# Performance work log

Measured on AMD Instinct MI355X. Metric: run time of the kernel, lower is better.

Reference implementation:

```python
import jax, jax.numpy as jnp
import numpy as np

# DeepSeek-V2 MLA dims (one tensor-parallel shard of 8)
H = 5120          # hidden size
S = 2048          # seq len
B = 1
NH = 16           # 128 heads / 8 devices
Q_LORA = 1536
KV_LORA = 512
NOPE = 128
ROPE = 64
QK = NOPE + ROPE  # 192 per-head q/k dim
VD = 128          # v head dim
DEVICE_NUM = 8
EPS = 1e-6


def rms_norm(x, w):
    v = jnp.mean(jnp.square(x.astype(jnp.float32)), axis=-1, keepdims=True)
    return (x * jax.lax.rsqrt(v + EPS)).astype(x.dtype) * w


def rope_cos_sin(position_ids, dim=ROPE, base=10000.0):
    inv_freq = 1.0 / (base ** (jnp.arange(0, dim, 2, dtype=jnp.float32) / dim))
    freqs = position_ids.astype(jnp.float32)[..., None] * inv_freq       # [B,S,dim/2]
    emb = jnp.concatenate([freqs, freqs], axis=-1)                        # [B,S,dim]
    return jnp.cos(emb), jnp.sin(emb)


def apply_rope(x, cos, sin):
    # DeepSeek interleaved reorder: view(b,h,s,d//2,2).transpose(-1,-2).reshape
    b, h, s, d = x.shape
    x = x.reshape(b, h, s, d // 2, 2).transpose(0, 1, 2, 4, 3).reshape(b, h, s, d)
    x1, x2 = x[..., : d // 2], x[..., d // 2:]
    rot = jnp.concatenate([-x2, x1], axis=-1)
    return x * cos[:, None] + rot * sin[:, None]


def setup_inputs() -> dict:
    key = jax.random.key(0)
    ks = jax.random.split(key, 8)
    sc = 0.02
    hidden_states = jax.random.normal(ks[0], (B, S, H), dtype=jnp.float32)
    position_ids = jnp.arange(S, dtype=jnp.int64 if jax.config.jax_enable_x64 else jnp.int32)[None, :].repeat(B, 0)
    attention_mask = jnp.triu(jnp.full((S, S), -1e9, dtype=jnp.float32), 1)[None, None]
    return {
        "hidden_states": hidden_states,
        "position_ids": position_ids,
        "attention_mask": attention_mask,
        "ln_w": jnp.ones((H,), jnp.float32),
        "q_a_w": jax.random.normal(ks[1], (Q_LORA, H), jnp.float32) * sc,
        "q_a_ln_w": jnp.ones((Q_LORA,), jnp.float32),
        "q_b_w": jax.random.normal(ks[2], (NH * QK, Q_LORA), jnp.float32) * sc,
        "kv_a_w": jax.random.normal(ks[3], (KV_LORA + ROPE, H), jnp.float32) * sc,
        "kv_a_ln_w": jnp.ones((KV_LORA,), jnp.float32),
        "kv_b_w": jax.random.normal(ks[4], (NH * (NOPE + VD), KV_LORA), jnp.float32) * sc,
        "o_w": jax.random.normal(ks[5], (H, NH * VD), jnp.float32) * sc,
    }


def reference(hidden_states, position_ids, attention_mask, ln_w, q_a_w, q_a_ln_w,
              q_b_w, kv_a_w, kv_a_ln_w, kv_b_w, o_w):
    b, s, _ = hidden_states.shape
    residual = hidden_states * (1.0 / DEVICE_NUM)
    x = rms_norm(hidden_states, ln_w)

    # Q path: low-rank down-proj + RMSNorm + up-proj
    q = rms_norm(x @ q_a_w.T, q_a_ln_w) @ q_b_w.T                # [b,s,NH*QK]
    q = q.reshape(b, s, NH, QK).transpose(0, 2, 1, 3)            # [b,NH,s,QK]
    q_nope, q_pe = q[..., :NOPE], q[..., NOPE:]

    # KV path: compressed latent + shared rope key
    ckv = x @ kv_a_w.T                                           # [b,s,KV_LORA+ROPE]
    c_kv, k_pe = ckv[..., :KV_LORA], ckv[..., KV_LORA:]
    k_pe = k_pe.reshape(b, s, 1, ROPE).transpose(0, 2, 1, 3)     # [b,1,s,ROPE]
    kv = rms_norm(c_kv, kv_a_ln_w) @ kv_b_w.T                    # [b,s,NH*(NOPE+VD)]
    kv = kv.reshape(b, s, NH, NOPE + VD).transpose(0, 2, 1, 3)
    k_nope, v = kv[..., :NOPE], kv[..., NOPE:]

    cos, sin = rope_cos_sin(position_ids)
    q_pe = apply_rope(q_pe, cos, sin)
    k_pe = apply_rope(k_pe, cos, sin)

    k = jnp.concatenate([k_nope, jnp.broadcast_to(k_pe, (b, NH, s, ROPE))], axis=-1)
    qf = jnp.concatenate([q_nope, q_pe], axis=-1)

    scores = jnp.einsum('bhqd,bhkd->bhqk', qf, k) * (1.0 / np.sqrt(QK))
    scores = scores + attention_mask
    probs = jax.nn.softmax(scores, axis=-1)
    attn = jnp.einsum('bhqk,bhkd->bhqd', probs, v)               # [b,NH,s,VD]

    out = attn.transpose(0, 2, 1, 3).reshape(b, s, NH * VD) @ o_w.T
    hidden = residual + out
    return hidden.astype(jnp.float32), k.astype(jnp.float32), v.astype(jnp.float32)
```

## Files before the change

kernel.cpp:

```cpp
#include <hip/hip_runtime.h>
#include <math.h>

typedef unsigned short u16;
typedef unsigned int u32;
typedef __attribute__((ext_vector_type(8))) short short8;
typedef __attribute__((ext_vector_type(4))) float f32x4;

#define NHEADS 16
static const int S      = 2048;
static const int Hd     = 5120;
static const int QLORA  = 1536;
static const int KVLORA = 512;
static const int NQK    = 192;
static const int NVD    = 128;
static const int QDIM   = 3072;
static const int KVDIM  = 4096;
static const int NFUSE  = 2176;

__device__ __forceinline__ u16 f2bf(float f) {
    union { float f; u32 u; } v; v.f = f;
    u32 r = v.u + 0x7FFFu + ((v.u >> 16) & 1u);
    return (u16)(r >> 16);
}
__device__ __forceinline__ float bf2f(u16 h) {
    union { u32 u; float f; } v; v.u = (u32)h << 16; return v.f;
}

__global__ void convert_bf16_kernel(const float* __restrict__ src, u16* __restrict__ dst,
                                    int n_src, int n_total) {
    int i = (blockIdx.x * 256 + threadIdx.x) * 4;
    if (i >= n_total) return;
    union { u16 h[4]; uint2 u; } p;
    if (i < n_src) {
        float4 v = *(const float4*)(src + i);
        p.h[0] = f2bf(v.x); p.h[1] = f2bf(v.y); p.h[2] = f2bf(v.z); p.h[3] = f2bf(v.w);
    } else {
        p.h[0] = p.h[1] = p.h[2] = p.h[3] = 0;
    }
    *(uint2*)(dst + i) = p.u;
}

__global__ void rmsnorm_bf16_kernel(const float* in, const float* __restrict__ w,
                                    u16* out, int D, int in_stride, int out_stride) {
    int row = blockIdx.x;
    const float* x = in + (size_t)row * in_stride;
    u16* y = out + (size_t)row * out_stride;
    float ss = 0.f;
    for (int i = threadIdx.x; i < D; i += blockDim.x) { float v = x[i]; ss += v * v; }
    #pragma unroll
    for (int off = 32; off > 0; off >>= 1) ss += __shfl_xor(ss, off);
    __shared__ float wsum[8];
    int wid = threadIdx.x >> 6, lane = threadIdx.x & 63;
    if (lane == 0) wsum[wid] = ss;
    __syncthreads();
    float tot = 0.f;
    int nw = blockDim.x >> 6;
    for (int i = 0; i < nw; ++i) tot += wsum[i];
    float scale = rsqrtf(tot / (float)D + 1e-6f);
    for (int i = threadIdx.x; i < D; i += blockDim.x) y[i] = f2bf(x[i] * scale * w[i]);
}

__global__ void rmsnorm_bf16in_kernel(const u16* in, const float* __restrict__ w,
                                      u16* out, int D, int in_stride, int out_stride) {
    int row = blockIdx.x;
    const u16* x = in + (size_t)row * in_stride;
    u16* y = out + (size_t)row * out_stride;
    float ss = 0.f;
    for (int i = threadIdx.x; i < D; i += blockDim.x) { float v = bf2f(x[i]); ss += v * v; }
    #pragma unroll
    for (int off = 32; off > 0; off >>= 1) ss += __shfl_xor(ss, off);
    __shared__ float wsum[8];
    int wid = threadIdx.x >> 6, lane = threadIdx.x & 63;
    if (lane == 0) wsum[wid] = ss;
    __syncthreads();
    float tot = 0.f;
    int nw = blockDim.x >> 6;
    for (int i = 0; i < nw; ++i) tot += wsum[i];
    float scale = rsqrtf(tot / (float)D + 1e-6f);
    for (int i = threadIdx.x; i < D; i += blockDim.x) y[i] = f2bf(bf2f(x[i]) * scale * w[i]);
}

template<int BM, bool SWZ, bool OBF, bool QPERM>
__global__ __launch_bounds__(256) void gemm_k(
    const u16* __restrict__ A, const u16* __restrict__ B, void* __restrict__ Cv,
    int M, int N, int K, const float* __restrict__ resid) {
    constexpr int MR = BM / 32;
    __shared__ u16 As[4][BM * 32];
    __shared__ u16 Bs[4][128 * 32];

    int bm, bn;
    if constexpr (SWZ) {
        const int lin = blockIdx.x + blockIdx.y * gridDim.x;
        const int nwg = gridDim.x * gridDim.y;
        const int xcd = lin & 7, off = lin >> 3;
        const int q = nwg >> 3, r = nwg & 7;
        const int wg = (xcd < r ? xcd * (q + 1) : r * (q + 1) + (xcd - r) * q) + off;
        bm = (wg % gridDim.y) * BM;
        bn = (wg / gridDim.y) * 128;
    } else {
        bm = blockIdx.y * BM;
        bn = blockIdx.x * 128;
    }

    const int tid = threadIdx.x;
    const int w = tid >> 6, lane = tid & 63;
    const int wr = w >> 1, wc = w & 1;
    const int fr = lane & 15, kg = lane >> 4;

    f32x4 acc[MR][4];
    #pragma unroll
    for (int i = 0; i < MR; ++i)
        #pragma unroll
        for (int j = 0; j < 4; ++j) acc[i][j] = (f32x4){0.f, 0.f, 0.f, 0.f};

    const int srow = lane >> 2;
    const int scol = (lane & 3) * 8;
    const u16* Ap0 = A + (size_t)(bm + w * (BM / 4) + srow) * K + scol;
    const u16* Ap1 = Ap0 + (size_t)16 * K;
    const u16* Bp0 = B + (size_t)(bn + w * 32 + srow) * K + scol;
    const u16* Bp1 = Bp0 + (size_t)16 * K;
    const int lda0 = (w * (BM / 4)) * 32;
    const int lda1 = (w * (BM / 4) + 16) * 32;
    const int ldb0 = (w * 32) * 32;
    const int ldb1 = (w * 32 + 16) * 32;

    auto STAGE = [&](int buf, int kk) {
        __builtin_amdgcn_global_load_lds(
            (const __attribute__((address_space(1))) void*)(Ap0 + kk),
            (__attribute__((address_space(3))) void*)&As[buf][lda0], 16, 0, 0);
        if constexpr (BM == 128)
            __builtin_amdgcn_global_load_lds(
                (const __attribute__((address_space(1))) void*)(Ap1 + kk),
                (__attribute__((address_space(3))) void*)&As[buf][lda1], 16, 0, 0);
        __builtin_amdgcn_global_load_lds(
            (const __attribute__((address_space(1))) void*)(Bp0 + kk),
            (__attribute__((address_space(3))) void*)&Bs[buf][ldb0], 16, 0, 0);
        __builtin_amdgcn_global_load_lds(
            (const __attribute__((address_space(1))) void*)(Bp1 + kk),
            (__attribute__((address_space(3))) void*)&Bs[buf][ldb1], 16, 0, 0);
    };
    auto COMP = [&](int buf) {
        short8 af[MR], bfr[4];
        #pragma unroll
        for (int i = 0; i < MR; ++i)
            af[i] = *(const short8*)&As[buf][(wr * (BM / 2) + i * 16 + fr) * 32 + kg * 8];
        #pragma unroll
        for (int i = 0; i < 4; ++i)
            bfr[i] = *(const short8*)&Bs[buf][(wc * 64 + i * 16 + fr) * 32 + kg * 8];
        #pragma unroll
        for (int mi = 0; mi < MR; ++mi)
            #pragma unroll
            for (int ni = 0; ni < 4; ++ni)
                acc[mi][ni] = __builtin_amdgcn_mfma_f32_16x16x32_bf16(af[mi], bfr[ni],
                                                                      acc[mi][ni], 0, 0, 0);
    };

    const int nk = K >> 5;
    STAGE(0, 0);
    STAGE(1, 32);
    for (int kt = 0; kt < nk; ++kt) {
        if (kt + 2 < nk) {
            STAGE((kt + 2) & 3, (kt + 2) << 5);
            if constexpr (BM == 128) asm volatile("s_waitcnt vmcnt(8)" ::: "memory");
            else                     asm volatile("s_waitcnt vmcnt(6)" ::: "memory");
        } else if (kt + 1 < nk) {
            if constexpr (BM == 128) asm volatile("s_waitcnt vmcnt(4)" ::: "memory");
            else                     asm volatile("s_waitcnt vmcnt(3)" ::: "memory");
        } else {
            asm volatile("s_waitcnt vmcnt(0)" ::: "memory");
        }
        __builtin_amdgcn_s_barrier();
        COMP(kt & 3);
    }

    #pragma unroll
    for (int mi = 0; mi < MR; ++mi)
        #pragma unroll
        for (int ni = 0; ni < 4; ++ni)
            #pragma unroll
            for (int r2 = 0; r2 < 4; ++r2) {
                int row = bm + wr * (BM / 2) + mi * 16 + kg * 4 + r2;
                int col = bn + wc * 64 + ni * 16 + fr;
                float v = acc[mi][ni][r2];
                if constexpr (QPERM) {
                    size_t idx = ((size_t)(col / 192) * S + row) * 192 + (col % 192);
                    ((u16*)Cv)[idx] = f2bf(v);
                } else if constexpr (OBF) {
                    ((u16*)Cv)[(size_t)row * N + col] = f2bf(v);
                } else {
                    size_t idx = (size_t)row * N + col;
                    if (resid) v += resid[idx] * 0.125f;
                    ((float*)Cv)[idx] = v;
                }
            }
}

__global__ void rope_q_inplace_kernel(u16* __restrict__ Qbf, const int* __restrict__ pos) {
    const int s = blockIdx.x;
    const int t = threadIdx.x;
    const int hh = t >> 5, j = t & 31;
    float ps = (float)pos[s];
    float inv_freq = 1.0f / powf(10000.0f, (float)j * (1.0f / 32.0f));
    float ang = ps * inv_freq;
    float c = cosf(ang), sn = sinf(ang);
    u16* base = Qbf + ((size_t)hh * S + s) * NQK;
    float a = bf2f(base[128 + 2 * j]), b = bf2f(base[128 + 2 * j + 1]);
    __syncthreads();
    base[128 + j] = f2bf(a * c - b * sn);
    base[160 + j] = f2bf(b * c + a * sn);
}

__global__ __launch_bounds__(256) void build_kv64_kernel(
    const u16* __restrict__ KVb, const u16* __restrict__ CF,
    const int* __restrict__ pos_ids,
    float* __restrict__ Kout, float* __restrict__ Vout,
    u16* __restrict__ Kbf, u16* __restrict__ Vtb) {
    const int s0 = blockIdx.x * 64;
    const int h  = blockIdx.y;
    const int t  = threadIdx.x;
    __shared__ u16 T[64][132];

    #pragma unroll
    for (int it = 0; it < 4; ++it) {
        int i = t + it * 256;
        int row = i >> 4, c8 = (i & 15) * 8;
        int s = s0 + row;
        union { uint4 u; u16 hx[8]; } v;
        v.u = *(const uint4*)(KVb + (size_t)s * KVDIM + h * 256 + c8);
        size_t kidx = ((size_t)h * S + s) * NQK + c8;
        *(uint4*)(Kbf + kidx) = v.u;
        float4 f0 = {bf2f(v.hx[0]), bf2f(v.hx[1]), bf2f(v.hx[2]), bf2f(v.hx[3])};
        float4 f1 = {bf2f(v.hx[4]), bf2f(v.hx[5]), bf2f(v.hx[6]), bf2f(v.hx[7])};
        *(float4*)(Kout + kidx) = f0;
        *(float4*)(Kout + kidx + 4) = f1;
    }
    #pragma unroll
    for (int it = 0; it < 4; ++it) {
        int i = t + it * 256;
        int row = i >> 4, c8 = (i & 15) * 8;
        int s = s0 + row;
        union { uint4 u; uint2 d[2]; u16 hx[8]; } v;
        v.u = *(const uint4*)(KVb + (size_t)s * KVDIM + h * 256 + 128 + c8);
        *(uint2*)&T[row][c8]     = v.d[0];
        *(uint2*)&T[row][c8 + 4] = v.d[1];
        size_t vidx = ((size_t)h * S + s) * NVD + c8;
        float4 f0 = {bf2f(v.hx[0]), bf2f(v.hx[1]), bf2f(v.hx[2]), bf2f(v.hx[3])};
        float4 f1 = {bf2f(v.hx[4]), bf2f(v.hx[5]), bf2f(v.hx[6]), bf2f(v.hx[7])};
        *(float4*)(Vout + vidx) = f0;
        *(float4*)(Vout + vidx + 4) = f1;
    }
    #pragma unroll
    for (int it = 0; it < 8; ++it) {
        int i = t + it * 256;
        int row = i >> 5, j = i & 31;
        int s = s0 + row;
        float ps = (float)pos_ids[s];
        float inv_freq = 1.0f / powf(10000.0f, (float)j * (1.0f / 32.0f));
        float ang = ps * inv_freq;
        float c = cosf(ang), sn = sinf(ang);
        u32 pr = *(const u32*)(CF + (size_t)s * NFUSE + QLORA + KVLORA + 2 * j);
        float a = bf2f((u16)pr), b = bf2f((u16)(pr >> 16));
        float k0 = a * c - b * sn;
        float k1 = b * c + a * sn;
        size_t kidx = ((size_t)h * S + s) * NQK;
        Kout[kidx + 128 + j] = k0;
        Kout[kidx + 160 + j] = k1;
        Kbf[kidx + 128 + j] = f2bf(k0);
        Kbf[kidx + 160 + j] = f2bf(k1);
    }
    __syncthreads();
    const int d = t >> 1, half = t & 1;
    #pragma unroll
    for (int c = 0; c < 4; ++c) {
        u16 tmp[8];
        #pragma unroll
        for (int e = 0; e < 8; ++e) tmp[e] = T[half * 32 + c * 8 + e][d];
        *(uint4*)(Vtb + ((size_t)h * NVD + d) * S + s0 + half * 32 + c * 8) = *(uint4*)tmp;
    }
}

__global__ __launch_bounds__(256) void attn_mfma_kernel(
    const u16* __restrict__ Qbf, const u16* __restrict__ Kb,
    const u16* __restrict__ Vtb, u16* __restrict__ ATb) {
    const int h = blockIdx.y;
    const int q0 = (gridDim.x - 1 - blockIdx.x) * 64;
    const int tid = threadIdx.x;
    const int w = tid >> 6, lane = tid & 63;
    const int fr = lane & 15, kg = lane >> 4;

    __shared__ __align__(16) u16 Ks[2][64 * 192];
    __shared__ __align__(16) u16 Vts[2][128 * 64];

    int kSrc[6], vSrc[4];
    #pragma unroll
    for (int i = 0; i < 6; ++i) {
        int D = (w * 6 + i) * 1024 + lane * 16;
        int row = D / 384, wb = D - row * 384;
        kSrc[i] = row * 384 + (wb ^ ((row & 7) << 4));
    }
    #pragma unroll
    for (int i = 0; i < 4; ++i) {
        int D = (w * 4 + i) * 1024 + lane * 16;
        int row = D >> 7, wb = D & 127;
        vSrc[i] = row * (S * 2) + (wb ^ ((row & 7) << 4));
    }
    const char* Kg = (const char*)(Kb + (size_t)h * S * NQK);
    const char* Vg = (const char*)(Vtb + (size_t)h * NVD * S);

    auto STAGE = [&](int buf, int kt) {
        const size_t krow = (size_t)kt * 64;
        #pragma unroll
        for (int i = 0; i < 6; ++i)
            __builtin_amdgcn_global_load_lds(
                (const __attribute__((address_space(1))) void*)(Kg + krow * 384 + kSrc[i]),
                (__attribute__((address_space(3))) void*)((char*)&Ks[buf][0] + (w * 6 + i) * 1024), 16, 0, 0);
        #pragma unroll
        for (int i = 0; i < 4; ++i)
            __builtin_amdgcn_global_load_lds(
                (const __attribute__((address_space(1))) void*)(Vg + krow * 2 + vSrc[i]),
                (__attribute__((address_space(3))) void*)((char*)&Vts[buf][0] + (w * 4 + i) * 1024), 16, 0, 0);
    };

    short8 qf[6];
    {
        const u16* qrow = Qbf + ((size_t)h * S + q0 + w * 16 + fr) * NQK;
        #pragma unroll
        for (int kb = 0; kb < 6; ++kb)
            qf[kb] = *(const short8*)(qrow + kb * 32 + kg * 8);
    }

    f32x4 o[8];
    #pragma unroll
    for (int ni = 0; ni < 8; ++ni) o[ni] = (f32x4){0.f, 0.f, 0.f, 0.f};
    float mrow = -1e30f, lrow = 0.f;
    const float scale = 0.0721687836487032f;
    const int qg = q0 + w * 16 + fr;
    const int swz = (fr & 7) << 4;
    const int nt = (q0 >> 6) + 1;

    STAGE(0, 0);
    asm volatile("s_waitcnt vmcnt(0)" ::: "memory");
    __builtin_amdgcn_s_barrier();

    for (int t = 0; t < nt; ++t) {
        if (t + 1 < nt) STAGE((t + 1) & 1, t + 1);
        const int buf = t & 1;
        const int k0 = t * 64;

        f32x4 sacc[4];
        #pragma unroll
        for (int mi = 0; mi < 4; ++mi) sacc[mi] = (f32x4){0.f, 0.f, 0.f, 0.f};
        __builtin_amdgcn_s_setprio(1);
        #pragma unroll
        for (int mi = 0; mi < 4; ++mi)
            #pragma unroll
            for (int kb = 0; kb < 6; ++kb) {
                const short8 kf = *(const short8*)((const char*)&Ks[buf][0] +
                    (mi * 16 + fr) * 384 + ((kb * 64 + kg * 16) ^ swz));
                sacc[mi] = __builtin_amdgcn_mfma_f32_16x16x32_bf16(kf, qf[kb], sacc[mi], 0, 0, 0);
            }
        __builtin_amdgcn_s_setprio(0);

        const bool diag = (k0 == q0);
        float p[4][4];
        float mx = -1e30f;
        #pragma unroll
        for (int mi = 0; mi < 4; ++mi)
            #pragma unroll
            for (int r = 0; r < 4; ++r) {
                float v = sacc[mi][r] * scale;
                if (diag && (k0 + mi * 16 + kg * 4 + r > qg)) v = -1e30f;
                p[mi][r] = v;
                mx = fmaxf(mx, v);
            }
        mx = fmaxf(mx, __shfl_xor(mx, 16));
        mx = fmaxf(mx, __shfl_xor(mx, 32));
        float mnew = fmaxf(mrow, mx);
        float corr = __expf(mrow - mnew);
        float psum = 0.f;
        #pragma unroll
        for (int mi = 0; mi < 4; ++mi)
            #pragma unroll
            for (int r = 0; r < 4; ++r) {
                float e = __expf(p[mi][r] - mnew);
                p[mi][r] = e;
                psum += e;
            }
        psum += __shfl_xor(psum, 16);
        psum += __shfl_xor(psum, 32);
        lrow = lrow * corr + psum;
        mrow = mnew;
        float corr_r[4];
        #pragma unroll
        for (int r = 0; r < 4; ++r) corr_r[r] = __shfl(corr, kg * 4 + r);
        #pragma unroll
        for (int ni = 0; ni < 8; ++ni) {
            o[ni][0] *= corr_r[0]; o[ni][1] *= corr_r[1];
            o[ni][2] *= corr_r[2]; o[ni][3] *= corr_r[3];
        }

        u32 pk0[4], pk1[4];
        #pragma unroll
        for (int mi = 0; mi < 4; ++mi) {
            pk0[mi] = (u32)f2bf(p[mi][0]) | ((u32)f2bf(p[mi][1]) << 16);
            pk1[mi] = (u32)f2bf(p[mi][2]) | ((u32)f2bf(p[mi][3]) << 16);
        }
        const int srcA = 2 * (kg & 1) * 16 + fr;
        const int srcB = srcA + 16;
        const int hsel = kg >> 1;
        short8 pa[2];
        #pragma unroll
        for (int ks = 0; ks < 2; ++ks) {
            u32 a0 = (u32)__shfl((int)pk0[ks * 2], srcA), b0 = (u32)__shfl((int)pk0[ks * 2 + 1], srcA);
            u32 a1 = (u32)__shfl((int)pk1[ks * 2], srcA), b1 = (u32)__shfl((int)pk1[ks * 2 + 1], srcA);
            u32 a2 = (u32)__shfl((int)pk0[ks * 2], srcB), b2 = (u32)__shfl((int)pk0[ks * 2 + 1], srcB);
            u32 a3 = (u32)__shfl((int)pk1[ks * 2], srcB), b3 = (u32)__shfl((int)pk1[ks * 2 + 1], srcB);
            union { u32 u[4]; short8 s8; } cvt;
            cvt.u[0] = hsel ? b0 : a0;
            cvt.u[1] = hsel ? b1 : a1;
            cvt.u[2] = hsel ? b2 : a2;
            cvt.u[3] = hsel ? b3 : a3;
            pa[ks] = cvt.s8;
        }

        __builtin_amdgcn_s_setprio(1);
        #pragma unroll
        for (int ks = 0; ks < 2; ++ks)
            #pragma unroll
            for (int ni = 0; ni < 8; ++ni) {
                const short8 vf = *(const short8*)((const char*)&Vts[buf][0] +
                    (ni * 16 + fr) * 128 + ((ks * 64 + kg * 16) ^ swz));
                o[ni] = __builtin_amdgcn_mfma_f32_16x16x32_bf16(pa[ks], vf, o[ni], 0, 0, 0);
            }
        __builtin_amdgcn_s_setprio(0);

        asm volatile("s_waitcnt vmcnt(0)" ::: "memory");
        __builtin_amdgcn_s_barrier();
    }

    float inv = 1.f / lrow;
    float inv_r[4];
    #pragma unroll
    for (int r = 0; r < 4; ++r) inv_r[r] = __shfl(inv, kg * 4 + r);
    u16* outp = ATb + (size_t)(q0 + w * 16 + kg * 4) * (NHEADS * NVD) + h * NVD + fr;
    #pragma unroll
    for (int ni = 0; ni < 8; ++ni)
        #pragma unroll
        for (int r = 0; r < 4; ++r)
            outp[(size_t)r * (NHEADS * NVD) + ni * 16] = f2bf(o[ni][r] * inv_r[r]);
}

extern "C" void kernel_launch(void* const* d_in, const int* in_sizes, int n_in,
                              void* d_out, int out_size, void* d_ws, size_t ws_size,
                              hipStream_t stream) {
    (void)in_sizes; (void)n_in; (void)out_size; (void)ws_size;
    const float* hidden    = (const float*)d_in[0];
    const int*   pos       = (const int*)d_in[1];
    const float* ln_w      = (const float*)d_in[3];
    const float* q_a_w     = (const float*)d_in[4];
    const float* q_a_ln_w  = (const float*)d_in[5];
    const float* q_b_w     = (const float*)d_in[6];
    const float* kv_a_w    = (const float*)d_in[7];
    const float* kv_a_ln_w = (const float*)d_in[8];
    const float* kv_b_w    = (const float*)d_in[9];
    const float* o_w       = (const float*)d_in[10];

    float* OUT_H = (float*)d_out;
    float* OUT_K = OUT_H + (size_t)S * Hd;
    float* OUT_V = OUT_K + (size_t)NHEADS * S * NQK;

    char* ws = (char*)d_ws;
    u16*   o_wb    = (u16*)(ws);
    u16*   Wf      = (u16*)(ws + 20971520);
    u16*   Qbf     = (u16*)(ws + 20971520);
    u16*   Vtb     = (u16*)(ws + 33554432);
    u16*   Xb      = (u16*)(ws + 43253760);
    u16*   Kbf     = (u16*)(ws + 43253760);
    u16*   ATb     = (u16*)(ws + 55836672);
    u16*   CF      = (u16*)(ws + 64225280);
    u16*   QAn     = (u16*)(ws + 73138176);
    u16*   CKVN    = (u16*)(ws + 73138176);
    u16*   q_b_wb  = (u16*)(ws + 79429632);
    u16*   kv_b_wb = (u16*)(ws + 79429632);
    u16*   KVb     = (u16*)(ws + 88866816);

    convert_bf16_kernel<<<(Hd * 2048 / 4 + 255) / 256, 256, 0, stream>>>(o_w, o_wb, Hd * 2048, Hd * 2048);
    convert_bf16_kernel<<<(QLORA * Hd / 4 + 255) / 256, 256, 0, stream>>>(q_a_w, Wf, QLORA * Hd, QLORA * Hd);
    convert_bf16_kernel<<<(640 * Hd / 4 + 255) / 256, 256, 0, stream>>>(kv_a_w, Wf + (size_t)QLORA * Hd, 576 * Hd, 640 * Hd);

    rmsnorm_bf16_kernel<<<S, 256, 0, stream>>>(hidden, ln_w, Xb, Hd, Hd, Hd);
    gemm_k<128, true, true, false><<<dim3(NFUSE / 128, S / 128), 256, 0, stream>>>(Xb, Wf, CF, S, NFUSE, Hd, nullptr);
    convert_bf16_kernel<<<(QDIM * QLORA / 4 + 255) / 256, 256, 0, stream>>>(q_b_w, q_b_wb, QDIM * QLORA, QDIM * QLORA);
    rmsnorm_bf16in_kernel<<<S, 256, 0, stream>>>(CF, q_a_ln_w, QAn, QLORA, NFUSE, QLORA);
    gemm_k<128, true, true, true><<<dim3(QDIM / 128, S / 128), 256, 0, stream>>>(QAn, q_b_wb, Qbf, S, QDIM, QLORA, nullptr);
    rope_q_inplace_kernel<<<S, 512, 0, stream>>>(Qbf, pos);
    convert_bf16_kernel<<<(KVDIM * KVLORA / 4 + 255) / 256, 256, 0, stream>>>(kv_b_w, kv_b_wb, KVDIM * KVLORA, KVDIM * KVLORA);
    rmsnorm_bf16in_kernel<<<S, 256, 0, stream>>>(CF + QLORA, kv_a_ln_w, CKVN, KVLORA, NFUSE, KVLORA);
    gemm_k<64, false, true, false><<<dim3(KVDIM / 128, S / 64), 256, 0, stream>>>(CKVN, kv_b_wb, KVb, S, KVDIM, KVLORA, nullptr);
    build_kv64_kernel<<<dim3(S / 64, NHEADS), 256, 0, stream>>>(KVb, CF, pos, OUT_K, OUT_V, Kbf, Vtb);
    attn_mfma_kernel<<<dim3(S / 64, NHEADS), 256, 0, stream>>>(Qbf, Kbf, Vtb, ATb);
    gemm_k<64, false, false, false><<<dim3(Hd / 128, S / 64), 256, 0, stream>>>(ATb, o_wb, OUT_H, S, Hd, NHEADS * NVD, hidden);
}
```

Measured before the change: 418.5 us.

## Use 256x256-tile 8-wave GEMM with interleaved LDS prefetch for output projection

Replaces the 64x128-tile GEMM for the o_proj with a new 512-thread kernel that computes 256x256 output tiles. It uses direct global-to-LDS loads into swizzled double buffers, split into four parts that are interleaved with four MFMA phases and raise wave priority around the MFMAs. The larger tiles give more reuse per byte loaded and overlap loads with compute. With only 20x8=160 blocks the grid is small for the device's CU count, so occupancy and tail effects are a risk, and the higher register use per thread adds pressure.

```diff
diff --git a/kernel.cpp b/kernel.cpp
--- a/kernel.cpp
+++ b/kernel.cpp
@@ -195,6 +195,112 @@
             }
 }
 
+#define QUAD8(MI, NI, A0, A1)                                                                 \
+    acc[MI][NI] = __builtin_amdgcn_mfma_f32_16x16x32_bf16(A0, bf[NI][0], acc[MI][NI], 0, 0, 0); \
+    acc[MI][NI] = __builtin_amdgcn_mfma_f32_16x16x32_bf16(A1, bf[NI][1], acc[MI][NI], 0, 0, 0);
+
+#define PHASE8(BUF, MI0) do {                                                                 \
+    const int ra0 = wr * 128 + (MI0) * 16 + fr;                                               \
+    const int ra1 = ra0 + 16;                                                                 \
+    short8 a00 = *(const short8*)((const char*)&As[BUF][0] + ra0 * 128 + ((kg * 16) ^ swz));  \
+    short8 a01 = *(const short8*)((const char*)&As[BUF][0] + ra0 * 128 + ((64 + kg * 16) ^ swz)); \
+    short8 a10 = *(const short8*)((const char*)&As[BUF][0] + ra1 * 128 + ((kg * 16) ^ swz));  \
+    short8 a11 = *(const short8*)((const char*)&As[BUF][0] + ra1 * 128 + ((64 + kg * 16) ^ swz)); \
+    __builtin_amdgcn_s_setprio(1);                                                            \
+    QUAD8(MI0, 0, a00, a01) QUAD8(MI0, 1, a00, a01)                                           \
+    QUAD8(MI0, 2, a00, a01) QUAD8(MI0, 3, a00, a01)                                           \
+    QUAD8(MI0 + 1, 0, a10, a11) QUAD8(MI0 + 1, 1, a10, a11)                                   \
+    QUAD8(MI0 + 1, 2, a10, a11) QUAD8(MI0 + 1, 3, a10, a11)                                   \
+    __builtin_amdgcn_s_setprio(0);                                                            \
+  } while (0)
+
+#define G8STAGE(BUF, KT, PART) do {                                                           \
+    const u16* Gp = ((PART) >= 2) ? A : B;                                                    \
+    const int hh = (PART) & 1;                                                                \
+    const int br = (((PART) >= 2) ? bm : bn) + hh * 128;                                      \
+    const char* gb = (const char*)(Gp + (size_t)br * K + (KT) * 64);                          \
+    u16* lb = ((PART) >= 2) ? &As[BUF][0] : &Bs[BUF][0];                                      \
+    __builtin_amdgcn_global_load_lds(                                                         \
+        (const __attribute__((address_space(1))) void*)(gb + (size_t)r0 * K2 + c0),           \
+        (__attribute__((address_space(3))) void*)((char*)lb + hh * 16384 + w * 1024), 16, 0, 0); \
+    __builtin_amdgcn_global_load_lds(                                                         \
+        (const __attribute__((address_space(1))) void*)(gb + (size_t)r1 * K2 + c1),           \
+        (__attribute__((address_space(3))) void*)((char*)lb + hh * 16384 + 8192 + w * 1024), 16, 0, 0); \
+  } while (0)
+
+__global__ __launch_bounds__(512, 2) void gemm8_kernel(
+    const u16* __restrict__ A, const u16* __restrict__ B, float* __restrict__ C,
+    int M, int N, int K, const float* __restrict__ resid) {
+    __shared__ u16 As[2][256 * 64];
+    __shared__ u16 Bs[2][256 * 64];
+    const int bm = blockIdx.y * 256, bn = blockIdx.x * 256;
+    const int tid = threadIdx.x;
+    const int w = tid >> 6, lane = tid & 63;
+    const int wr = w >> 2, wc = w & 3;
+    const int fr = lane & 15, kg = lane >> 4;
+    const int swz = (fr & 7) << 4;
+
+    f32x4 acc[8][4];
+    #pragma unroll
+    for (int i = 0; i < 8; ++i)
+        #pragma unroll
+        for (int j = 0; j < 4; ++j) acc[i][j] = (f32x4){0.f, 0.f, 0.f, 0.f};
+
+    const int D0 = tid * 16, D1 = 8192 + tid * 16;
+    const int r0 = D0 >> 7; const int c0 = (D0 & 127) ^ ((r0 & 7) << 4);
+    const int r1 = D1 >> 7; const int c1 = (D1 & 127) ^ ((r1 & 7) << 4);
+    const size_t K2 = (size_t)K * 2;
+
+    const int nk = K >> 6;
+    G8STAGE(0, 0, 0); G8STAGE(0, 0, 1); G8STAGE(0, 0, 2); G8STAGE(0, 0, 3);
+
+    short8 bf[4][2];
+    for (int kt = 0; kt < nk; ++kt) {
+        const int b = kt & 1;
+        const bool pre = (kt + 1 < nk);
+        asm volatile("" ::: "memory");
+        if (pre) {
+            G8STAGE(b ^ 1, kt + 1, 0);
+            asm volatile("s_waitcnt vmcnt(2)" ::: "memory");
+        } else {
+            asm volatile("s_waitcnt vmcnt(0)" ::: "memory");
+        }
+        __builtin_amdgcn_s_barrier();
+        asm volatile("" ::: "memory");
+        #pragma unroll
+        for (int ni = 0; ni < 4; ++ni) {
+            const int rb = wc * 64 + ni * 16 + fr;
+            bf[ni][0] = *(const short8*)((const char*)&Bs[b][0] + rb * 128 + ((kg * 16) ^ swz));
+            bf[ni][1] = *(const short8*)((const char*)&Bs[b][0] + rb * 128 + ((64 + kg * 16) ^ swz));
+        }
+        if (pre) G8STAGE(b ^ 1, kt + 1, 1);
+        PHASE8(b, 0);
+        __builtin_amdgcn_s_barrier();
+        if (pre) G8STAGE(b ^ 1, kt + 1, 2);
+        PHASE8(b, 2);
+        __builtin_amdgcn_s_barrier();
+        if (pre) G8STAGE(b ^ 1, kt + 1, 3);
+        PHASE8(b, 4);
+        __builtin_amdgcn_s_barrier();
+        PHASE8(b, 6);
+        __builtin_amdgcn_s_barrier();
+    }
+
+    #pragma unroll
+    for (int mi = 0; mi < 8; ++mi)
+        #pragma unroll
+        for (int ni = 0; ni < 4; ++ni)
+            #pragma unroll
+            for (int r2 = 0; r2 < 4; ++r2) {
+                int row = bm + wr * 128 + mi * 16 + kg * 4 + r2;
+                int col = bn + wc * 64 + ni * 16 + fr;
+                size_t idx = (size_t)row * N + col;
+                float v = acc[mi][ni][r2];
+                if (resid) v += resid[idx] * 0.125f;
+                C[idx] = v;
+            }
+}
+
 __global__ void rope_q_inplace_kernel(u16* __restrict__ Qbf, const int* __restrict__ pos) {
     const int s = blockIdx.x;
     const int t = threadIdx.x;
@@ -499,5 +605,5 @@
     gemm_k<64, false, true, false><<<dim3(KVDIM / 128, S / 64), 256, 0, stream>>>(CKVN, kv_b_wb, KVb, S, KVDIM, KVLORA, nullptr);
     build_kv64_kernel<<<dim3(S / 64, NHEADS), 256, 0, stream>>>(KVb, CF, pos, OUT_K, OUT_V, Kbf, Vtb);
     attn_mfma_kernel<<<dim3(S / 64, NHEADS), 256, 0, stream>>>(Qbf, Kbf, Vtb, ATb);
-    gemm_k<64, false, false, false><<<dim3(Hd / 128, S / 64), 256, 0, stream>>>(ATb, o_wb, OUT_H, S, Hd, NHEADS * NVD, hidden);
-}
+    gemm8_kernel<<<dim3(Hd / 256, S / 256), 512, 0, stream>>>(ATb, o_wb, OUT_H, S, Hd, NHEADS * NVD, hidden);
+}
```

New measurement: 443.4 us. 1.06x slower.

## Merge weight conversions, q/kv rmsnorms, and q/kv up-projection GEMMs into single launches

Applied to the files above, without the earlier changes.

Replaces five separate fp32-to-bf16 weight conversion launches with one kernel that dispatches on a flat chunk index, and merges the q and kv latent RMSNorms into one 2D-grid launch. The q_b and kv_b up-projection GEMMs become one grouped kernel, where blocks with x<24 compute Q and the rest compute KV, all using 64-row tiles. Workspace offsets are moved so CKVN, q_b_wb, kv_b_wb and KVb no longer alias, which lets the merged work coexist. The aim is to cut launch count and tail underutilisation from the small GEMMs. The cost is that the Q GEMM drops from a swizzled 128-row tile to an unswizzled 64-row tile, which may lower its efficiency.

```diff
diff --git a/kernel.cpp b/kernel.cpp
--- a/kernel.cpp
+++ b/kernel.cpp
@@ -26,18 +26,29 @@
     union { u32 u; float f; } v; v.u = (u32)h << 16; return v.f;
 }
 
-__global__ void convert_bf16_kernel(const float* __restrict__ src, u16* __restrict__ dst,
-                                    int n_src, int n_total) {
-    int i = (blockIdx.x * 256 + threadIdx.x) * 4;
-    if (i >= n_total) return;
+__global__ void convert_all_kernel(const float* __restrict__ o_w,
+                                   const float* __restrict__ q_a_w,
+                                   const float* __restrict__ kv_a_w,
+                                   const float* __restrict__ q_b_w,
+                                   const float* __restrict__ kv_b_w,
+                                   u16* __restrict__ o_wb, u16* __restrict__ Wf,
+                                   u16* __restrict__ q_b_wb, u16* __restrict__ kv_b_wb) {
+    long c = (long)blockIdx.x * 256 + threadIdx.x;
+    const float* src; u16* dst; long nsrcc;
+    if (c < 2621440L)      { src = o_w;    dst = o_wb;            nsrcc = 2621440L; }
+    else if (c < 4587520L) { c -= 2621440L; src = q_a_w; dst = Wf; nsrcc = 1966080L; }
+    else if (c < 5406720L) { c -= 4587520L; src = kv_a_w; dst = Wf + 7864320L; nsrcc = 737280L; }
+    else if (c < 6586368L) { c -= 5406720L; src = q_b_w;  dst = q_b_wb;  nsrcc = 1179648L; }
+    else if (c < 7110656L) { c -= 6586368L; src = kv_b_w; dst = kv_b_wb; nsrcc = 524288L; }
+    else return;
     union { u16 h[4]; uint2 u; } p;
-    if (i < n_src) {
-        float4 v = *(const float4*)(src + i);
+    if (c < nsrcc) {
+        float4 v = *(const float4*)(src + c * 4);
         p.h[0] = f2bf(v.x); p.h[1] = f2bf(v.y); p.h[2] = f2bf(v.z); p.h[3] = f2bf(v.w);
     } else {
         p.h[0] = p.h[1] = p.h[2] = p.h[3] = 0;
     }
-    *(uint2*)(dst + i) = p.u;
+    *(uint2*)(dst + c * 4) = p.u;
 }
 
 __global__ void rmsnorm_bf16_kernel(const float* in, const float* __restrict__ w,
@@ -60,22 +71,27 @@
     for (int i = threadIdx.x; i < D; i += blockDim.x) y[i] = f2bf(x[i] * scale * w[i]);
 }
 
-__global__ void rmsnorm_bf16in_kernel(const u16* in, const float* __restrict__ w,
-                                      u16* out, int D, int in_stride, int out_stride) {
-    int row = blockIdx.x;
-    const u16* x = in + (size_t)row * in_stride;
-    u16* y = out + (size_t)row * out_stride;
+__global__ void rms_qkv_kernel(const u16* __restrict__ CF,
+                               const float* __restrict__ qw, const float* __restrict__ kw,
+                               u16* __restrict__ QAn, u16* __restrict__ CKVN) {
+    const int row = blockIdx.x;
+    const u16* x; u16* y; const float* w; int D;
+    if (blockIdx.y == 0) {
+        x = CF + (size_t)row * NFUSE;          y = QAn + (size_t)row * QLORA;
+        w = qw; D = QLORA;
+    } else {
+        x = CF + (size_t)row * NFUSE + QLORA;  y = CKVN + (size_t)row * KVLORA;
+        w = kw; D = KVLORA;
+    }
     float ss = 0.f;
     for (int i = threadIdx.x; i < D; i += blockDim.x) { float v = bf2f(x[i]); ss += v * v; }
     #pragma unroll
     for (int off = 32; off > 0; off >>= 1) ss += __shfl_xor(ss, off);
-    __shared__ float wsum[8];
+    __shared__ float wsum[4];
     int wid = threadIdx.x >> 6, lane = threadIdx.x & 63;
     if (lane == 0) wsum[wid] = ss;
     __syncthreads();
-    float tot = 0.f;
-    int nw = blockDim.x >> 6;
-    for (int i = 0; i < nw; ++i) tot += wsum[i];
+    float tot = wsum[0] + wsum[1] + wsum[2] + wsum[3];
     float scale = rsqrtf(tot / (float)D + 1e-6f);
     for (int i = threadIdx.x; i < D; i += blockDim.x) y[i] = f2bf(bf2f(x[i]) * scale * w[i]);
 }
@@ -195,6 +211,100 @@
             }
 }
 
+__global__ __launch_bounds__(256) void gemm_qkv_kernel(
+    const u16* __restrict__ QAn, const u16* __restrict__ CKVN,
+    const u16* __restrict__ q_b_wb, const u16* __restrict__ kv_b_wb,
+    u16* __restrict__ Qbf, u16* __restrict__ KVb) {
+    __shared__ u16 As[4][64 * 32];
+    __shared__ u16 Bs[4][128 * 32];
+    const bool isQ = blockIdx.x < 24;
+    const u16* A = isQ ? QAn : CKVN;
+    const u16* B = isQ ? q_b_wb : kv_b_wb;
+    const int K = isQ ? QLORA : KVLORA;
+    const int bn = (isQ ? blockIdx.x : blockIdx.x - 24) * 128;
+    const int bm = blockIdx.y * 64;
+
+    const int tid = threadIdx.x;
+    const int w = tid >> 6, lane = tid & 63;
+    const int wr = w >> 1, wc = w & 1;
+    const int fr = lane & 15, kg = lane >> 4;
+
+    f32x4 acc[2][4];
+    #pragma unroll
+    for (int i = 0; i < 2; ++i)
+        #pragma unroll
+        for (int j = 0; j < 4; ++j) acc[i][j] = (f32x4){0.f, 0.f, 0.f, 0.f};
+
+    const int srow = lane >> 2;
+    const int scol = (lane & 3) * 8;
+    const u16* Ap0 = A + (size_t)(bm + w * 16 + srow) * K + scol;
+    const u16* Bp0 = B + (size_t)(bn + w * 32 + srow) * K + scol;
+    const u16* Bp1 = Bp0 + (size_t)16 * K;
+    const int lda0 = (w * 16) * 32;
+    const int ldb0 = (w * 32) * 32;
+    const int ldb1 = (w * 32 + 16) * 32;
+
+    auto STAGE = [&](int buf, int kk) {
+        __builtin_amdgcn_global_load_lds(
+            (const __attribute__((address_space(1))) void*)(Ap0 + kk),
+            (__attribute__((address_space(3))) void*)&As[buf][lda0], 16, 0, 0);
+        __builtin_amdgcn_global_load_lds(
+            (const __attribute__((address_space(1))) void*)(Bp0 + kk),
+            (__attribute__((address_space(3))) void*)&Bs[buf][ldb0], 16, 0, 0);
+        __builtin_amdgcn_global_load_lds(
+            (const __attribute__((address_space(1))) void*)(Bp1 + kk),
+            (__attribute__((address_space(3))) void*)&Bs[buf][ldb1], 16, 0, 0);
+    };
+    auto COMP = [&](int buf) {
+        short8 af[2], bfr[4];
+        #pragma unroll
+        for (int i = 0; i < 2; ++i)
+            af[i] = *(const short8*)&As[buf][(wr * 32 + i * 16 + fr) * 32 + kg * 8];
+        #pragma unroll
+        for (int i = 0; i < 4; ++i)
+            bfr[i] = *(const short8*)&Bs[buf][(wc * 64 + i * 16 + fr) * 32 + kg * 8];
+        #pragma unroll
+        for (int mi = 0; mi < 2; ++mi)
+            #pragma unroll
+            for (int ni = 0; ni < 4; ++ni)
+                acc[mi][ni] = __builtin_amdgcn_mfma_f32_16x16x32_bf16(af[mi], bfr[ni],
+                                                                      acc[mi][ni], 0, 0, 0);
+    };
+
+    const int nk = K >> 5;
+    STAGE(0, 0);
+    STAGE(1, 32);
+    for (int kt = 0; kt < nk; ++kt) {
+        if (kt + 2 < nk) {
+            STAGE((kt + 2) & 3, (kt + 2) << 5);
+            asm volatile("s_waitcnt vmcnt(6)" ::: "memory");
+        } else if (kt + 1 < nk) {
+            asm volatile("s_waitcnt vmcnt(3)" ::: "memory");
+        } else {
+            asm volatile("s_waitcnt vmcnt(0)" ::: "memory");
+        }
+        __builtin_amdgcn_s_barrier();
+        COMP(kt & 3);
+    }
+
+    #pragma unroll
+    for (int mi = 0; mi < 2; ++mi)
+        #pragma unroll
+        for (int ni = 0; ni < 4; ++ni)
+            #pragma unroll
+            for (int r2 = 0; r2 < 4; ++r2) {
+                int row = bm + wr * 32 + mi * 16 + kg * 4 + r2;
+                int col = bn + wc * 64 + ni * 16 + fr;
+                float v = acc[mi][ni][r2];
+                if (isQ) {
+                    size_t idx = ((size_t)(col / 192) * S + row) * 192 + (col % 192);
+                    Qbf[idx] = f2bf(v);
+                } else {
+                    KVb[(size_t)row * KVDIM + col] = f2bf(v);
+                }
+            }
+}
+
 __global__ void rope_q_inplace_kernel(u16* __restrict__ Qbf, const int* __restrict__ pos) {
     const int s = blockIdx.x;
     const int t = threadIdx.x;
@@ -479,24 +589,18 @@
     u16*   ATb     = (u16*)(ws + 55836672);
     u16*   CF      = (u16*)(ws + 64225280);
     u16*   QAn     = (u16*)(ws + 73138176);
-    u16*   CKVN    = (u16*)(ws + 73138176);
-    u16*   q_b_wb  = (u16*)(ws + 79429632);
-    u16*   kv_b_wb = (u16*)(ws + 79429632);
-    u16*   KVb     = (u16*)(ws + 88866816);
-
-    convert_bf16_kernel<<<(Hd * 2048 / 4 + 255) / 256, 256, 0, stream>>>(o_w, o_wb, Hd * 2048, Hd * 2048);
-    convert_bf16_kernel<<<(QLORA * Hd / 4 + 255) / 256, 256, 0, stream>>>(q_a_w, Wf, QLORA * Hd, QLORA * Hd);
-    convert_bf16_kernel<<<(640 * Hd / 4 + 255) / 256, 256, 0, stream>>>(kv_a_w, Wf + (size_t)QLORA * Hd, 576 * Hd, 640 * Hd);
-
+    u16*   CKVN    = (u16*)(ws + 79429632);
+    u16*   q_b_wb  = (u16*)(ws + 81526784);
+    u16*   kv_b_wb = (u16*)(ws + 90963968);
+    u16*   KVb     = (u16*)(ws + 95158272);
+
+    convert_all_kernel<<<27776, 256, 0, stream>>>(o_w, q_a_w, kv_a_w, q_b_w, kv_b_w,
+                                                  o_wb, Wf, q_b_wb, kv_b_wb);
     rmsnorm_bf16_kernel<<<S, 256, 0, stream>>>(hidden, ln_w, Xb, Hd, Hd, Hd);
     gemm_k<128, true, true, false><<<dim3(NFUSE / 128, S / 128), 256, 0, stream>>>(Xb, Wf, CF, S, NFUSE, Hd, nullptr);
-    convert_bf16_kernel<<<(QDIM * QLORA / 4 + 255) / 256, 256, 0, stream>>>(q_b_w, q_b_wb, QDIM * QLORA, QDIM * QLORA);
-    rmsnorm_bf16in_kernel<<<S, 256, 0, stream>>>(CF, q_a_ln_w, QAn, QLORA, NFUSE, QLORA);
-    gemm_k<128, true, true, true><<<dim3(QDIM / 128, S / 128), 256, 0, stream>>>(QAn, q_b_wb, Qbf, S, QDIM, QLORA, nullptr);
+    rms_qkv_kernel<<<dim3(S, 2), 256, 0, stream>>>(CF, q_a_ln_w, kv_a_ln_w, QAn, CKVN);
+    gemm_qkv_kernel<<<dim3(56, S / 64), 256, 0, stream>>>(QAn, CKVN, q_b_wb, kv_b_wb, Qbf, KVb);
     rope_q_inplace_kernel<<<S, 512, 0, stream>>>(Qbf, pos);
-    convert_bf16_kernel<<<(KVDIM * KVLORA / 4 + 255) / 256, 256, 0, stream>>>(kv_b_w, kv_b_wb, KVDIM * KVLORA, KVDIM * KVLORA);
-    rmsnorm_bf16in_kernel<<<S, 256, 0, stream>>>(CF + QLORA, kv_a_ln_w, CKVN, KVLORA, NFUSE, KVLORA);
-    gemm_k<64, false, true, false><<<dim3(KVDIM / 128, S / 64), 256, 0, stream>>>(CKVN, kv_b_wb, KVb, S, KVDIM, KVLORA, nullptr);
     build_kv64_kernel<<<dim3(S / 64, NHEADS), 256, 0, stream>>>(KVb, CF, pos, OUT_K, OUT_V, Kbf, Vtb);
     attn_mfma_kernel<<<dim3(S / 64, NHEADS), 256, 0, stream>>>(Qbf, Kbf, Vtb, ATb);
     gemm_k<64, false, false, false><<<dim3(Hd / 128, S / 64), 256, 0, stream>>>(ATb, o_wb, OUT_H, S, Hd, NHEADS * NVD, hidden);
```

Result: no change. 412.3 us (median of 2 runs) (-1.5%).
